# Performance work log

Hardware: AMD Instinct MI355X
Metric: run time of the kernel (lower is better)

The kernel has to match this reference:

```python
import jax, jax.numpy as jnp
import numpy as np

N_NODES = 100000
N_EDGES = 1600000
D_IN = 128
D_HID = 128
D_OUT = 128
N_GRAPHS = 64


def setup_inputs() -> dict:
    key = jax.random.key(0)
    ks = jax.random.split(key, 10)
    x = jax.random.normal(ks[0], (N_NODES, D_IN), dtype=jnp.float32)
    edge_index = jax.random.randint(ks[1], (2, N_EDGES), 0, N_NODES, dtype=jnp.int64)
    graph_id = jnp.sort(jax.random.randint(ks[2], (N_NODES,), 0, N_GRAPHS, dtype=jnp.int64))
    s1 = 1.0 / np.sqrt(D_IN)
    s2 = 1.0 / np.sqrt(D_HID)
    s3 = 1.0 / np.sqrt(D_OUT)
    W1 = jax.random.normal(ks[3], (D_IN, D_HID), dtype=jnp.float32) * s1
    b1 = jnp.zeros((D_HID,), dtype=jnp.float32)
    W2 = jax.random.normal(ks[4], (D_HID, D_OUT), dtype=jnp.float32) * s2
    b2 = jnp.zeros((D_OUT,), dtype=jnp.float32)
    Wr1 = jax.random.normal(ks[5], (D_OUT, D_OUT), dtype=jnp.float32) * s3
    br1 = jnp.zeros((D_OUT,), dtype=jnp.float32)
    Wr2 = jax.random.normal(ks[6], (D_OUT, D_OUT), dtype=jnp.float32) * s3
    br2 = jnp.zeros((D_OUT,), dtype=jnp.float32)
    return {"x": x, "edge_index": edge_index, "graph_id": graph_id,
            "num_graphs": N_GRAPHS, "W1": W1, "b1": b1, "W2": W2, "b2": b2,
            "Wr1": Wr1, "br1": br1, "Wr2": Wr2, "br2": br2}


def _graph_conv(h, W, b, src, dst, norm_src, norm_dst, n_nodes):
    # DGL GraphConv, norm='both': out = D_dst^{-1/2} A (D_src^{-1/2} h) W + b
    h = h * norm_src[:, None]
    h = h @ W  # project first (cheap, keeps SpMM on the smaller/equal dim)
    agg = jax.ops.segment_sum(h[src], dst, num_segments=n_nodes)
    return agg * norm_dst[:, None] + b


def reference(x, edge_index, graph_id, num_graphs, W1, b1, W2, b2, Wr1, br1, Wr2, br2):
    src, dst = edge_index[0], edge_index[1]
    n_nodes = x.shape[0]
    ones = jnp.ones((src.shape[0],), dtype=x.dtype)
    deg_out = jax.ops.segment_sum(ones, src, num_segments=n_nodes)
    deg_in = jax.ops.segment_sum(ones, dst, num_segments=n_nodes)
    norm_src = jnp.clip(deg_out, 1.0) ** -0.5
    norm_dst = jnp.clip(deg_in, 1.0) ** -0.5

    # layer 1 + relu (dropout is identity in eval mode)
    h = _graph_conv(x, W1, b1, src, dst, norm_src, norm_dst, n_nodes)
    h = jax.nn.relu(h)
    # layer 2 + relu
    h = _graph_conv(h, W2, b2, src, dst, norm_src, norm_dst, n_nodes)
    h = jax.nn.relu(h)

    # per-graph mean pooling (dgl.mean_nodes)
    sums = jax.ops.segment_sum(h, graph_id, num_segments=num_graphs)
    counts = jax.ops.segment_sum(jnp.ones((n_nodes,), dtype=h.dtype), graph_id,
                                 num_segments=num_graphs)
    hg = sums / jnp.clip(counts, 1.0)[:, None]

    # readout MLP: Linear -> ReLU -> Linear
    out = jax.nn.relu(hg @ Wr1 + br1) @ Wr2 + br2
    return (out, h)
```

## Files before the change

### kernel.cpp

```cpp
#include <hip/hip_runtime.h>
#include <math.h>


#define D 128
#define BSH 9
#define BSZ 512

typedef _Float16 half8 __attribute__((ext_vector_type(8)));
typedef _Float16 half4v __attribute__((ext_vector_type(4)));
typedef _Float16 half2v __attribute__((ext_vector_type(2)));
typedef float f32x4 __attribute__((ext_vector_type(4)));

union H8 { half8 v; half2v h[4]; };

__global__ __launch_bounds__(256) void k_coarse(const int* __restrict__ src,
                                                const int* __restrict__ dst,
                                                int* __restrict__ cnt_d,
                                                int* __restrict__ cnt_s,
                                                int* __restrict__ blkbase_d,
                                                int* __restrict__ blkbase_s,
                                                int E, int nbkt) {
  __shared__ int hd[256], hs[256];
  int t = threadIdx.x;
  hd[t] = 0; hs[t] = 0;
  __syncthreads();
  int chunk = (E + gridDim.x - 1) / gridDim.x;
  int lo = blockIdx.x * chunk, hi = min(lo + chunk, E);
  for (int e = lo + t; e < hi; e += 256) {
    atomicAdd(&hd[dst[e] >> BSH], 1);
    atomicAdd(&hs[src[e] >> BSH], 1);
  }
  __syncthreads();
  if (t < nbkt) {
    int c = hd[t];
    blkbase_d[blockIdx.x * 256 + t] = c ? atomicAdd(&cnt_d[t], c) : 0;
    c = hs[t];
    blkbase_s[blockIdx.x * 256 + t] = c ? atomicAdd(&cnt_s[t], c) : 0;
  }
}

__global__ __launch_bounds__(256) void k_cscan(const int* __restrict__ cnt_d,
                                               const int* __restrict__ cnt_s,
                                               int* __restrict__ ptr_d,
                                               int* __restrict__ ptr_s,
                                               const int* __restrict__ gid,
                                               int* __restrict__ gptr,
                                               int nbkt, int E, int N) {
  __shared__ int sh[256];
  int t = threadIdx.x;
  int v = (t < nbkt) ? cnt_d[t] : 0;
  sh[t] = v;
  __syncthreads();
  for (int off = 1; off < 256; off <<= 1) {
    int a = (t >= off) ? sh[t - off] : 0;
    __syncthreads();
    sh[t] += a;
    __syncthreads();
  }
  if (t < nbkt) ptr_d[t] = sh[t] - v;
  if (t == 0) ptr_d[nbkt] = E;
  __syncthreads();
  v = (t < nbkt) ? cnt_s[t] : 0;
  sh[t] = v;
  __syncthreads();
  for (int off = 1; off < 256; off <<= 1) {
    int a = (t >= off) ? sh[t - off] : 0;
    __syncthreads();
    sh[t] += a;
    __syncthreads();
  }
  if (t < nbkt) ptr_s[t] = sh[t] - v;
  if (t == 0) ptr_s[nbkt] = E;
  if (t <= 64) {
    int lo = 0, hi = N;
    while (lo < hi) {
      int m = (lo + hi) >> 1;
      if (gid[m] < t) lo = m + 1; else hi = m;
    }
    gptr[t] = lo;
  }
}

__global__ __launch_bounds__(256) void k_cscatter(const int* __restrict__ src,
                                                  const int* __restrict__ dst,
                                                  const int* __restrict__ ptr_d,
                                                  const int* __restrict__ ptr_s,
                                                  const int* __restrict__ blkbase_d,
                                                  const int* __restrict__ blkbase_s,
                                                  int* __restrict__ packed_d,
                                                  int* __restrict__ packed_s,
                                                  int E, int nbkt) {
  __shared__ int hd[256], hs[256], bd[256], bs2[256];
  int t = threadIdx.x;
  if (t < nbkt) {
    bd[t]  = ptr_d[t] + blkbase_d[blockIdx.x * 256 + t];
    bs2[t] = ptr_s[t] + blkbase_s[blockIdx.x * 256 + t];
  }
  hd[t] = 0; hs[t] = 0;
  __syncthreads();
  int chunk = (E + gridDim.x - 1) / gridDim.x;
  int lo = blockIdx.x * chunk, hi = min(lo + chunk, E);
  for (int e = lo + t; e < hi; e += 256) {
    int s = src[e], d = dst[e];
    int b1 = d >> BSH;
    int r1 = atomicAdd(&hd[b1], 1);
    packed_d[bd[b1] + r1] = ((d & (BSZ - 1)) << 17) | s;
    int b2 = s >> BSH;
    int r2 = atomicAdd(&hs[b2], 1);
    packed_s[bs2[b2] + r2] = s & (BSZ - 1);
  }
}

__global__ __launch_bounds__(256) void k_fine_dst(const int* __restrict__ packed_d,
                                                  const int* __restrict__ ptr_d,
                                                  int* __restrict__ row_end,
                                                  int* __restrict__ csr, int N) {
  __shared__ int hist[512], excl[512], ps[256];
  int b = blockIdx.x, t = threadIdx.x;
  int lo = ptr_d[b], hi = ptr_d[b + 1];
  hist[t] = 0; hist[t + 256] = 0;
  __syncthreads();
  for (int e = lo + t; e < hi; e += 256)
    atomicAdd(&hist[packed_d[e] >> 17], 1);
  __syncthreads();
  int a0 = hist[2 * t], a1 = hist[2 * t + 1];
  ps[t] = a0 + a1;
  __syncthreads();
  for (int off = 1; off < 256; off <<= 1) {
    int a = (t >= off) ? ps[t - off] : 0;
    __syncthreads();
    ps[t] += a;
    __syncthreads();
  }
  int exc = ps[t] - (a0 + a1);
  excl[2 * t] = exc;
  excl[2 * t + 1] = exc + a0;
  int nbase = b << BSH;
  if (nbase + 2 * t < N)     row_end[nbase + 2 * t]     = lo + exc + a0;
  if (nbase + 2 * t + 1 < N) row_end[nbase + 2 * t + 1] = lo + exc + a0 + a1;
  __syncthreads();
  hist[t] = 0; hist[t + 256] = 0;
  __syncthreads();
  for (int e = lo + t; e < hi; e += 256) {
    int p = packed_d[e];
    int dlow = p >> 17, s = p & 0x1FFFF;
    int r = atomicAdd(&hist[dlow], 1);
    csr[lo + excl[dlow] + r] = s;
  }
}

__global__ __launch_bounds__(256) void k_fine_src(const int* __restrict__ packed_s,
                                                  const int* __restrict__ ptr_s,
                                                  float* __restrict__ norm_src, int N) {
  __shared__ int hist[512];
  int b = blockIdx.x, t = threadIdx.x;
  int lo = ptr_s[b], hi = ptr_s[b + 1];
  hist[t] = 0; hist[t + 256] = 0;
  __syncthreads();
  for (int e = lo + t; e < hi; e += 256)
    atomicAdd(&hist[packed_s[e]], 1);
  __syncthreads();
  int nbase = b << BSH;
  for (int i = t; i < BSZ; i += 256)
    if (nbase + i < N)
      norm_src[nbase + i] = rsqrtf(fmaxf((float)hist[i], 1.0f));
}

__global__ __launch_bounds__(256) void k_prep(const float* __restrict__ W1,
                                              const float* __restrict__ W2,
                                              _Float16* __restrict__ Wt1,
                                              _Float16* __restrict__ Wt2) {
  int idx = blockIdx.x * 256 + threadIdx.x;
  int m = idx >> 14;
  int i = idx & 16383;
  int k = i >> 7, n = i & 127;
  const float* W = m ? W2 : W1;
  _Float16* Wt = m ? Wt2 : Wt1;
  Wt[n * 128 + k] = (_Float16)W[i];
}

__global__ __launch_bounds__(256) void k_gemm1(const float* __restrict__ A,
                                               const _Float16* __restrict__ Wt,
                                               const float* __restrict__ scale,
                                               _Float16* __restrict__ C, int N) {
  __shared__ _Float16 As[64][136];
  __shared__ _Float16 Cs[64][128];
  const int r0 = blockIdx.x * 64;
  const int t = threadIdx.x;
  for (int i = t; i < 64 * 32; i += 256) {
    int r = i >> 5, c4 = i & 31;
    float4 v = {0.f, 0.f, 0.f, 0.f};
    if (r0 + r < N) {
      v = ((const float4*)A)[(size_t)(r0 + r) * 32 + c4];
      float s = scale[r0 + r];
      v.x *= s; v.y *= s; v.z *= s; v.w *= s;
    }
    half4v h = {(_Float16)v.x, (_Float16)v.y, (_Float16)v.z, (_Float16)v.w};
    *(half4v*)&As[r][c4 * 4] = h;
  }
  __syncthreads();
  const int w = t >> 6, l = t & 63;
  const int c = l & 15, quad = l >> 4;
  f32x4 acc[8];
#pragma unroll
  for (int nt = 0; nt < 8; ++nt) acc[nt] = (f32x4){0.f, 0.f, 0.f, 0.f};
#pragma unroll
  for (int kc = 0; kc < 4; ++kc) {
    half8 a = *(const half8*)&As[w * 16 + c][kc * 32 + quad * 8];
#pragma unroll
    for (int nt = 0; nt < 8; ++nt) {
      half8 b = *(const half8*)&Wt[(size_t)(nt * 16 + c) * 128 + kc * 32 + quad * 8];
      acc[nt] = __builtin_amdgcn_mfma_f32_16x16x32_f16(a, b, acc[nt], 0, 0, 0);
    }
  }
#pragma unroll
  for (int nt = 0; nt < 8; ++nt)
#pragma unroll
    for (int r = 0; r < 4; ++r)
      Cs[w * 16 + quad * 4 + r][nt * 16 + c] = (_Float16)acc[nt][r];
  __syncthreads();
  for (int i = t; i < 64 * 16; i += 256) {
    int r = i >> 4, c8 = i & 15;
    if (r0 + r < N)
      ((half8*)C)[(size_t)(r0 + r) * 16 + c8] = *(half8*)&Cs[r][c8 * 8];
  }
}

__global__ __launch_bounds__(256) void k_gemm2(const _Float16* __restrict__ A,
                                               const _Float16* __restrict__ Wt,
                                               _Float16* __restrict__ C, int N) {
  __shared__ _Float16 As[64][136];
  __shared__ _Float16 Cs[64][128];
  const int r0 = blockIdx.x * 64;
  const int t = threadIdx.x;
  for (int i = t; i < 64 * 16; i += 256) {
    int r = i >> 4, c8 = i & 15;
    half8 v = {0, 0, 0, 0, 0, 0, 0, 0};
    if (r0 + r < N) v = ((const half8*)A)[(size_t)(r0 + r) * 16 + c8];
    *(half8*)&As[r][c8 * 8] = v;
  }
  __syncthreads();
  const int w = t >> 6, l = t & 63;
  const int c = l & 15, quad = l >> 4;
  f32x4 acc[8];
#pragma unroll
  for (int nt = 0; nt < 8; ++nt) acc[nt] = (f32x4){0.f, 0.f, 0.f, 0.f};
#pragma unroll
  for (int kc = 0; kc < 4; ++kc) {
    half8 a = *(const half8*)&As[w * 16 + c][kc * 32 + quad * 8];
#pragma unroll
    for (int nt = 0; nt < 8; ++nt) {
      half8 b = *(const half8*)&Wt[(size_t)(nt * 16 + c) * 128 + kc * 32 + quad * 8];
      acc[nt] = __builtin_amdgcn_mfma_f32_16x16x32_f16(a, b, acc[nt], 0, 0, 0);
    }
  }
#pragma unroll
  for (int nt = 0; nt < 8; ++nt)
#pragma unroll
    for (int r = 0; r < 4; ++r)
      Cs[w * 16 + quad * 4 + r][nt * 16 + c] = (_Float16)acc[nt][r];
  __syncthreads();
  for (int i = t; i < 64 * 16; i += 256) {
    int r = i >> 4, c8 = i & 15;
    if (r0 + r < N)
      ((half8*)C)[(size_t)(r0 + r) * 16 + c8] = *(half8*)&Cs[r][c8 * 8];
  }
}

#define FDOT2_ROW(u)                                                        \
  _Pragma("unroll")                                                         \
  for (int k = 0; k < 4; ++k) {                                             \
    acc[2 * k]     = __builtin_amdgcn_fdot2((u).h[k], c10, acc[2 * k], false); \
    acc[2 * k + 1] = __builtin_amdgcn_fdot2((u).h[k], c01, acc[2 * k + 1], false); \
  }

__device__ __forceinline__ void gather_core(const half8* __restrict__ P8,
                                            const int* __restrict__ csr,
                                            int start, int end, int cg, int eg,
                                            int lane, float* acc) {
  const half2v c10 = {(_Float16)1.0f, (_Float16)0.0f};
  const half2v c01 = {(_Float16)0.0f, (_Float16)1.0f};
  for (int s0 = start; s0 < end; s0 += 64) {
    int cnt = min(64, end - s0);
    int idx = (s0 + lane < end) ? csr[s0 + lane] : 0;
    int base = 0;
    for (; base + 16 <= cnt; base += 16) {
      int i0 = __shfl(idx, base + eg);
      int i1 = __shfl(idx, base + 4 + eg);
      int i2 = __shfl(idx, base + 8 + eg);
      int i3 = __shfl(idx, base + 12 + eg);
      H8 u0, u1, u2, u3;
      u0.v = P8[(size_t)i0 * 16 + cg];
      u1.v = P8[(size_t)i1 * 16 + cg];
      u2.v = P8[(size_t)i2 * 16 + cg];
      u3.v = P8[(size_t)i3 * 16 + cg];
      FDOT2_ROW(u0) FDOT2_ROW(u1) FDOT2_ROW(u2) FDOT2_ROW(u3)
    }
    for (; base + 4 <= cnt; base += 4) {
      int i0 = __shfl(idx, base + eg);
      H8 u0;
      u0.v = P8[(size_t)i0 * 16 + cg];
      FDOT2_ROW(u0)
    }
    if (base < cnt) {
      int j = min(base + eg, cnt - 1);
      int i0 = __shfl(idx, j);
      if (base + eg < cnt) {
        H8 u0;
        u0.v = P8[(size_t)i0 * 16 + cg];
        FDOT2_ROW(u0)
      }
    }
  }
#pragma unroll
  for (int j = 0; j < 8; ++j) {
    acc[j] += __shfl_xor(acc[j], 16);
    acc[j] += __shfl_xor(acc[j], 32);
  }
}

__global__ __launch_bounds__(256) void k_gather1(const half8* __restrict__ P8,
                                                 const int* __restrict__ row_end,
                                                 const int* __restrict__ csr,
                                                 const float* __restrict__ bias,
                                                 const float* __restrict__ norm_src,
                                                 half2v* __restrict__ outH, int N) {
  int wid = (blockIdx.x * 256 + threadIdx.x) >> 6;
  if (wid >= N) return;
  int lane = threadIdx.x & 63;
  int cg = lane & 15, eg = lane >> 4;
  int end = row_end[wid];
  int start = (wid == 0) ? 0 : row_end[wid - 1];
  float acc[8] = {0.f, 0.f, 0.f, 0.f, 0.f, 0.f, 0.f, 0.f};
  gather_core(P8, csr, start, end, cg, eg, lane, acc);
  float nd = rsqrtf(fmaxf((float)(end - start), 1.0f));
  float ns = norm_src[wid];
  float2 b = ((const float2*)bias)[cg * 4 + eg];
  half2v o = {(_Float16)(fmaxf(acc[eg * 2] * nd + b.x, 0.f) * ns),
              (_Float16)(fmaxf(acc[eg * 2 + 1] * nd + b.y, 0.f) * ns)};
  outH[(size_t)wid * 64 + cg * 4 + eg] = o;
}

__global__ __launch_bounds__(256) void k_gather2(const half8* __restrict__ P8,
                                                 const int* __restrict__ row_end,
                                                 const int* __restrict__ csr,
                                                 const float* __restrict__ bias,
                                                 float2* __restrict__ outH, int N) {
  int wid = (blockIdx.x * 256 + threadIdx.x) >> 6;
  if (wid >= N) return;
  int lane = threadIdx.x & 63;
  int cg = lane & 15, eg = lane >> 4;
  int end = row_end[wid];
  int start = (wid == 0) ? 0 : row_end[wid - 1];
  float acc[8] = {0.f, 0.f, 0.f, 0.f, 0.f, 0.f, 0.f, 0.f};
  gather_core(P8, csr, start, end, cg, eg, lane, acc);
  float nd = rsqrtf(fmaxf((float)(end - start), 1.0f));
  float2 b = ((const float2*)bias)[cg * 4 + eg];
  float2 o;
  o.x = fmaxf(acc[eg * 2] * nd + b.x, 0.f);
  o.y = fmaxf(acc[eg * 2 + 1] * nd + b.y, 0.f);
  outH[(size_t)wid * 64 + cg * 4 + eg] = o;
}

__global__ __launch_bounds__(256) void k_pool(const float* __restrict__ H,
                                              const int* __restrict__ gptr,
                                              float* __restrict__ pool) {
  int g = blockIdx.x >> 3, chunk = blockIdx.x & 7;
  int col = threadIdx.x & 127, rpar = threadIdx.x >> 7;
  int s = gptr[g], e = gptr[g + 1];
  float acc = 0.0f;
  for (int r = s + chunk * 2 + rpar; r < e; r += 16)
    acc += H[(size_t)r * D + col];
  __shared__ float red[256];
  red[threadIdx.x] = acc;
  __syncthreads();
  if (rpar == 0) atomicAdd(&pool[g * D + col], acc + red[threadIdx.x + 128]);
}

__global__ __launch_bounds__(128) void k_readout(const float* __restrict__ pool,
                                                 const int* __restrict__ gptr,
                                                 const float* __restrict__ Wr1,
                                                 const float* __restrict__ br1,
                                                 const float* __restrict__ Wr2,
                                                 const float* __restrict__ br2,
                                                 float* __restrict__ out) {
  int g = blockIdx.x;
  int j = threadIdx.x;
  __shared__ float hg[D];
  __shared__ float t1[D];
  float cnt = fmaxf((float)(gptr[g + 1] - gptr[g]), 1.0f);
  hg[j] = pool[(size_t)g * D + j] / cnt;
  __syncthreads();
  float a = br1[j];
  for (int k = 0; k < D; ++k) a += hg[k] * Wr1[(size_t)k * D + j];
  t1[j] = fmaxf(a, 0.0f);
  __syncthreads();
  float b = br2[j];
  for (int k = 0; k < D; ++k) b += t1[k] * Wr2[(size_t)k * D + j];
  out[(size_t)g * D + j] = b;
}

extern "C" void kernel_launch(void* const* d_in, const int* in_sizes, int n_in,
                              void* d_out, int out_size, void* d_ws, size_t ws_size,
                              hipStream_t stream) {
  const float* x   = (const float*)d_in[0];
  const int* edge  = (const int*)d_in[1];
  const int* gid   = (const int*)d_in[2];
  const float* W1  = (const float*)d_in[4];
  const float* b1  = (const float*)d_in[5];
  const float* W2  = (const float*)d_in[6];
  const float* b2  = (const float*)d_in[7];
  const float* Wr1 = (const float*)d_in[8];
  const float* br1 = (const float*)d_in[9];
  const float* Wr2 = (const float*)d_in[10];
  const float* br2 = (const float*)d_in[11];

  const int N = in_sizes[0] / D;
  const int E = in_sizes[1] / 2;
  const int* src = edge;
  const int* dst = edge + E;
  const int nbkt = (N + BSZ - 1) >> BSH;

  float* bufA     = (float*)d_ws;
  float* bufB     = bufA + (size_t)N * D;
  int* row_end    = (int*)(bufB + (size_t)N * D);
  int* csr        = row_end + N;
  float* norm_src = (float*)(csr + E);
  float* pool     = norm_src + N;
  int* gptr       = (int*)(pool + 64 * D);
  int* cnt_d      = gptr + 65;
  int* cnt_s      = cnt_d + 256;
  int* ptr_d      = cnt_s + 256;
  int* ptr_s      = ptr_d + 257;
  _Float16* Wt1   = (_Float16*)(ptr_s + 257);
  _Float16* Wt2   = Wt1 + 128 * 128;
  int* packed_d   = (int*)bufA;
  int* packed_s   = packed_d + E;
  int* blkbase_d  = packed_s + E;
  int* blkbase_s  = blkbase_d + 256 * 256;
  size_t need = ((size_t)2 * N * D + 2 * N + E + 64 * D + 65 + 1026 + 8192)
                * sizeof(float);
  if (ws_size < need) return;

  float* out_g = (float*)d_out;
  float* h_out = out_g + 64 * D;

  _Float16* P   = (_Float16*)bufA;
  _Float16* h1p = (_Float16*)bufB;

  hipMemsetAsync(cnt_d, 0, 512 * sizeof(int), stream);
  hipMemsetAsync(pool, 0, 64 * D * sizeof(float), stream);

  k_prep<<<128, 256, 0, stream>>>(W1, W2, Wt1, Wt2);

  k_coarse<<<256, 256, 0, stream>>>(src, dst, cnt_d, cnt_s, blkbase_d, blkbase_s, E, nbkt);
  k_cscan<<<1, 256, 0, stream>>>(cnt_d, cnt_s, ptr_d, ptr_s, gid, gptr, nbkt, E, N);
  k_cscatter<<<256, 256, 0, stream>>>(src, dst, ptr_d, ptr_s, blkbase_d, blkbase_s,
                                      packed_d, packed_s, E, nbkt);
  k_fine_dst<<<nbkt, 256, 0, stream>>>(packed_d, ptr_d, row_end, csr, N);
  k_fine_src<<<nbkt, 256, 0, stream>>>(packed_s, ptr_s, norm_src, N);

  const int gemm_grid = (N + 63) / 64;

  k_gemm1<<<gemm_grid, 256, 0, stream>>>(x, Wt1, norm_src, P, N);
  k_gather1<<<(N * 64 + 255) / 256, 256, 0, stream>>>(
      (const half8*)P, row_end, csr, b1, norm_src, (half2v*)h1p, N);

  k_gemm2<<<gemm_grid, 256, 0, stream>>>(h1p, Wt2, P, N);
  k_gather2<<<(N * 64 + 255) / 256, 256, 0, stream>>>(
      (const half8*)P, row_end, csr, b2, (float2*)h_out, N);

  k_pool<<<64 * 8, 256, 0, stream>>>(h_out, gptr, pool);
  k_readout<<<64, 128, 0, stream>>>(pool, gptr, Wr1, br1, Wr2, br2, out_g);
}
```

Before: 423.8 us.

## Merge fine-sort kernels, fold memsets into prep, accumulate gathers in packed fp16

The two fine bucket-sort kernels become one launch that splits its blocks between the dst-CSR build and the src-degree count. The two memsets move into an extra block of the weight-prep kernel, so there are fewer launches and API calls. The gather inner loop now sums neighbor rows with packed half2 adds instead of fdot2 into fp32 accumulators, halving the ALU work per row. That change accumulates in fp16, which for rows with about 16 neighbors risks rounding error and possible overflow compared with fp32.

```diff
diff --git a/kernel.cpp b/kernel.cpp
--- a/kernel.cpp
+++ b/kernel.cpp
@@ -111,12 +111,31 @@
   }
 }
 
-__global__ __launch_bounds__(256) void k_fine_dst(const int* __restrict__ packed_d,
-                                                  const int* __restrict__ ptr_d,
-                                                  int* __restrict__ row_end,
-                                                  int* __restrict__ csr, int N) {
+__global__ __launch_bounds__(256) void k_fine(const int* __restrict__ packed_d,
+                                              const int* __restrict__ ptr_d,
+                                              int* __restrict__ row_end,
+                                              int* __restrict__ csr,
+                                              const int* __restrict__ packed_s,
+                                              const int* __restrict__ ptr_s,
+                                              float* __restrict__ norm_src,
+                                              int N, int nbkt) {
   __shared__ int hist[512], excl[512], ps[256];
-  int b = blockIdx.x, t = threadIdx.x;
+  int t = threadIdx.x;
+  if (blockIdx.x >= nbkt) {
+    int b = blockIdx.x - nbkt;
+    int lo = ptr_s[b], hi = ptr_s[b + 1];
+    hist[t] = 0; hist[t + 256] = 0;
+    __syncthreads();
+    for (int e = lo + t; e < hi; e += 256)
+      atomicAdd(&hist[packed_s[e]], 1);
+    __syncthreads();
+    int nbase = b << BSH;
+    for (int i = t; i < BSZ; i += 256)
+      if (nbase + i < N)
+        norm_src[nbase + i] = rsqrtf(fmaxf((float)hist[i], 1.0f));
+    return;
+  }
+  int b = blockIdx.x;
   int lo = ptr_d[b], hi = ptr_d[b + 1];
   hist[t] = 0; hist[t + 256] = 0;
   __syncthreads();
@@ -149,27 +168,18 @@
   }
 }
 
-__global__ __launch_bounds__(256) void k_fine_src(const int* __restrict__ packed_s,
-                                                  const int* __restrict__ ptr_s,
-                                                  float* __restrict__ norm_src, int N) {
-  __shared__ int hist[512];
-  int b = blockIdx.x, t = threadIdx.x;
-  int lo = ptr_s[b], hi = ptr_s[b + 1];
-  hist[t] = 0; hist[t + 256] = 0;
-  __syncthreads();
-  for (int e = lo + t; e < hi; e += 256)
-    atomicAdd(&hist[packed_s[e]], 1);
-  __syncthreads();
-  int nbase = b << BSH;
-  for (int i = t; i < BSZ; i += 256)
-    if (nbase + i < N)
-      norm_src[nbase + i] = rsqrtf(fmaxf((float)hist[i], 1.0f));
-}
-
 __global__ __launch_bounds__(256) void k_prep(const float* __restrict__ W1,
                                               const float* __restrict__ W2,
                                               _Float16* __restrict__ Wt1,
-                                              _Float16* __restrict__ Wt2) {
+                                              _Float16* __restrict__ Wt2,
+                                              int* __restrict__ cnt_d,
+                                              float* __restrict__ pool) {
+  if (blockIdx.x == 128) {
+    int t = threadIdx.x;
+    cnt_d[t] = 0; cnt_d[t + 256] = 0;
+    for (int i = t; i < 64 * D; i += 256) pool[i] = 0.0f;
+    return;
+  }
   int idx = blockIdx.x * 256 + threadIdx.x;
   int m = idx >> 14;
   int i = idx & 16383;
@@ -267,19 +277,16 @@
   }
 }
 
-#define FDOT2_ROW(u)                                                        \
+#define PK_ROW(u)                                                           \
   _Pragma("unroll")                                                         \
-  for (int k = 0; k < 4; ++k) {                                             \
-    acc[2 * k]     = __builtin_amdgcn_fdot2((u).h[k], c10, acc[2 * k], false); \
-    acc[2 * k + 1] = __builtin_amdgcn_fdot2((u).h[k], c01, acc[2 * k + 1], false); \
-  }
+  for (int k = 0; k < 4; ++k) acch[k] += (u).h[k];
 
 __device__ __forceinline__ void gather_core(const half8* __restrict__ P8,
                                             const int* __restrict__ csr,
                                             int start, int end, int cg, int eg,
                                             int lane, float* acc) {
-  const half2v c10 = {(_Float16)1.0f, (_Float16)0.0f};
-  const half2v c01 = {(_Float16)0.0f, (_Float16)1.0f};
+  half2v acch[4] = {{(_Float16)0.f, (_Float16)0.f}, {(_Float16)0.f, (_Float16)0.f},
+                    {(_Float16)0.f, (_Float16)0.f}, {(_Float16)0.f, (_Float16)0.f}};
   for (int s0 = start; s0 < end; s0 += 64) {
     int cnt = min(64, end - s0);
     int idx = (s0 + lane < end) ? csr[s0 + lane] : 0;
@@ -294,13 +301,13 @@
       u1.v = P8[(size_t)i1 * 16 + cg];
       u2.v = P8[(size_t)i2 * 16 + cg];
       u3.v = P8[(size_t)i3 * 16 + cg];
-      FDOT2_ROW(u0) FDOT2_ROW(u1) FDOT2_ROW(u2) FDOT2_ROW(u3)
+      PK_ROW(u0) PK_ROW(u1) PK_ROW(u2) PK_ROW(u3)
     }
     for (; base + 4 <= cnt; base += 4) {
       int i0 = __shfl(idx, base + eg);
       H8 u0;
       u0.v = P8[(size_t)i0 * 16 + cg];
-      FDOT2_ROW(u0)
+      PK_ROW(u0)
     }
     if (base < cnt) {
       int j = min(base + eg, cnt - 1);
@@ -308,9 +315,14 @@
       if (base + eg < cnt) {
         H8 u0;
         u0.v = P8[(size_t)i0 * 16 + cg];
-        FDOT2_ROW(u0)
+        PK_ROW(u0)
       }
     }
+  }
+#pragma unroll
+  for (int k = 0; k < 4; ++k) {
+    acc[2 * k]     = (float)acch[k].x;
+    acc[2 * k + 1] = (float)acch[k].y;
   }
 #pragma unroll
   for (int j = 0; j < 8; ++j) {
@@ -331,7 +343,7 @@
   int cg = lane & 15, eg = lane >> 4;
   int end = row_end[wid];
   int start = (wid == 0) ? 0 : row_end[wid - 1];
-  float acc[8] = {0.f, 0.f, 0.f, 0.f, 0.f, 0.f, 0.f, 0.f};
+  float acc[8];
   gather_core(P8, csr, start, end, cg, eg, lane, acc);
   float nd = rsqrtf(fmaxf((float)(end - start), 1.0f));
   float ns = norm_src[wid];
@@ -352,7 +364,7 @@
   int cg = lane & 15, eg = lane >> 4;
   int end = row_end[wid];
   int start = (wid == 0) ? 0 : row_end[wid - 1];
-  float acc[8] = {0.f, 0.f, 0.f, 0.f, 0.f, 0.f, 0.f, 0.f};
+  float acc[8];
   gather_core(P8, csr, start, end, cg, eg, lane, acc);
   float nd = rsqrtf(fmaxf((float)(end - start), 1.0f));
   float2 b = ((const float2*)bias)[cg * 4 + eg];
@@ -448,17 +460,14 @@
   _Float16* P   = (_Float16*)bufA;
   _Float16* h1p = (_Float16*)bufB;
 
-  hipMemsetAsync(cnt_d, 0, 512 * sizeof(int), stream);
-  hipMemsetAsync(pool, 0, 64 * D * sizeof(float), stream);
-
-  k_prep<<<128, 256, 0, stream>>>(W1, W2, Wt1, Wt2);
+  k_prep<<<129, 256, 0, stream>>>(W1, W2, Wt1, Wt2, cnt_d, pool);
 
   k_coarse<<<256, 256, 0, stream>>>(src, dst, cnt_d, cnt_s, blkbase_d, blkbase_s, E, nbkt);
   k_cscan<<<1, 256, 0, stream>>>(cnt_d, cnt_s, ptr_d, ptr_s, gid, gptr, nbkt, E, N);
   k_cscatter<<<256, 256, 0, stream>>>(src, dst, ptr_d, ptr_s, blkbase_d, blkbase_s,
                                       packed_d, packed_s, E, nbkt);
-  k_fine_dst<<<nbkt, 256, 0, stream>>>(packed_d, ptr_d, row_end, csr, N);
-  k_fine_src<<<nbkt, 256, 0, stream>>>(packed_s, ptr_s, norm_src, N);
+  k_fine<<<2 * nbkt, 256, 0, stream>>>(packed_d, ptr_d, row_end, csr,
+                                       packed_s, ptr_s, norm_src, N, nbkt);
 
   const int gemm_grid = (N + 63) / 64;
 
```

Result: faster. 406.7 us (-4.0%).
